# Kernel optimization log

Hardware: AMD Instinct MI355X
Metric: run time of the kernel (lower is better)

## Reference

```python
import jax, jax.numpy as jnp
import numpy as np

N = 50000
E = 800000
D = 16            # input_dim == hidden_dim == output_dim (required for consistency)
D2 = D * D
HEADS = 4
NEG_SLOPE = 0.2


def _gat_conv(x, src, dst, W, att_src, att_dst, bias):
    """PyG GATConv with concat=False (mean over heads), add_self_loops already applied.
    x: [N, Cin], W: [Cin, H*C], att_*: [H, C], bias: [C]."""
    H, C = att_src.shape
    xh = (x @ W).reshape(N, H, C)                     # [N, H, C]
    a_src = jnp.einsum('nhc,hc->nh', xh, att_src)      # [N, H]
    a_dst = jnp.einsum('nhc,hc->nh', xh, att_dst)
    alpha = jax.nn.leaky_relu(a_src[src] + a_dst[dst], NEG_SLOPE)   # [E, H]
    amax = jax.ops.segment_max(alpha, dst, num_segments=N)
    amax = jnp.where(jnp.isfinite(amax), amax, 0.0)
    ex = jnp.exp(alpha - jax.lax.stop_gradient(amax)[dst])
    denom = jax.ops.segment_sum(ex, dst, num_segments=N)
    coef = ex / (denom[dst] + 1e-16)                  # per-dst softmax over incoming edges
    acc = jnp.zeros((N, C), x.dtype)
    for h in range(H):  # loop over heads to avoid [E, H, C] intermediate
        acc = acc + jax.ops.segment_sum(coef[:, h:h + 1] * xh[src, h], dst, num_segments=N)
    return acc / H + bias


def setup_inputs() -> dict:
    key = jax.random.key(0)
    ks = jax.random.split(key, 20)
    s = lambda k, shape, fan: jax.random.normal(k, shape, jnp.float32) * (1.0 / np.sqrt(fan))
    inp = {
        'mean': jax.random.normal(ks[0], (N, D), jnp.float32),
        'cov': jax.random.normal(ks[1], (N, D, D), jnp.float32),
        'edge_index': jax.random.randint(ks[2], (2, E), 0, N, jnp.int32),
        # gat_mean params
        'W_mean': s(ks[3], (D, HEADS * D), D),
        'att_src_mean': s(ks[4], (HEADS, D), D),
        'att_dst_mean': s(ks[5], (HEADS, D), D),
        'bias_mean': jnp.zeros((D,), jnp.float32),
        # gat_cov params
        'W_cov': s(ks[6], (D2, HEADS * D2), D2),
        'att_src_cov': s(ks[7], (HEADS, D2), D2),
        'att_dst_cov': s(ks[8], (HEADS, D2), D2),
        'bias_cov': jnp.zeros((D2,), jnp.float32),
        # fc_mean: Linear(D,D) -> Linear(D,D)
        'fm_W1': s(ks[9], (D, D), D), 'fm_b1': jnp.zeros((D,), jnp.float32),
        'fm_W2': s(ks[10], (D, D), D), 'fm_b2': jnp.zeros((D,), jnp.float32),
        # fc_cov: Linear(D2,D2) -> Linear(D2,D2)
        'fcv_W1': s(ks[11], (D2, D2), D2), 'fcv_b1': jnp.zeros((D2,), jnp.float32),
        'fcv_W2': s(ks[12], (D2, D2), D2), 'fcv_b2': jnp.zeros((D2,), jnp.float32),
    }
    return inp


def reference(mean, cov, edge_index, W_mean, att_src_mean, att_dst_mean, bias_mean,
              W_cov, att_src_cov, att_dst_cov, bias_cov,
              fm_W1, fm_b1, fm_W2, fm_b2, fcv_W1, fcv_b1, fcv_W2, fcv_b2):
    loops = jnp.arange(N, dtype=edge_index.dtype)
    src = jnp.concatenate([edge_index[0], loops])
    dst = jnp.concatenate([edge_index[1], loops])

    cov_flat = cov.reshape(N, D2)
    mean_agg = _gat_conv(mean, src, dst, W_mean, att_src_mean, att_dst_mean, bias_mean)
    cov_agg = _gat_conv(cov_flat, src, dst, W_cov, att_src_cov, att_dst_cov, bias_cov)

    mean_out = (mean_agg @ fm_W1 + fm_b1) @ fm_W2 + fm_b2
    cov_out = (cov_agg @ fcv_W1 + fcv_b1) @ fcv_W2 + fcv_b2
    return mean_out, cov_out.reshape(N, D, D)
```

## Files before the change

kernel.cpp:

```cpp
#include <hip/hip_runtime.h>

#define NN 50000
#define EE 800000
#define DD 16
#define DD2 256
#define ETOT (EE + NN)
#define NB 196

typedef __bf16 bf16x8 __attribute__((ext_vector_type(8)));
typedef float f32x4 __attribute__((ext_vector_type(4)));
typedef float f32x2 __attribute__((ext_vector_type(2)));

__device__ inline unsigned short f2bf(float f) {
    unsigned int u = __float_as_uint(f);
    return (unsigned short)((u + 0x7FFFu + ((u >> 16) & 1u)) >> 16);
}

__device__ inline void gl2lds16(const void* g, void* l) {
    __builtin_amdgcn_global_load_lds((const __attribute__((address_space(1))) unsigned int*)g,
                                     (__attribute__((address_space(3))) unsigned int*)l, 16, 0, 0);
}

__global__ void k_count(const int* ei, int* counts) {
    int e = blockIdx.x * 256 + threadIdx.x;
    if (e < EE) atomicAdd(&counts[ei[EE + e]], 1);
}

__global__ void k_scan1(const int* counts, int* partial, int* bsum) {
    __shared__ int sh[256];
    int t = threadIdx.x;
    int n = blockIdx.x * 256 + t;
    int v = (n < NN) ? counts[n] + 1 : 0;
    sh[t] = v;
    __syncthreads();
    for (int d = 1; d < 256; d <<= 1) {
        int x = (t >= d) ? sh[t - d] : 0;
        __syncthreads();
        sh[t] += x;
        __syncthreads();
    }
    if (n < NN) partial[n] = sh[t];
    if (t == 255) bsum[blockIdx.x] = sh[255];
}

__global__ void k_scan3(const int* counts, const int* partial, const int* bsum,
                        int* row_start, int* cursor) {
    __shared__ int sh[256];
    int t = threadIdx.x;
    int v = (t < NB) ? bsum[t] : 0;
    sh[t] = v;
    __syncthreads();
    for (int d = 1; d < 256; d <<= 1) {
        int x = (t >= d) ? sh[t - d] : 0;
        __syncthreads();
        sh[t] += x;
        __syncthreads();
    }
    int boff = (blockIdx.x == 0) ? 0 : sh[blockIdx.x - 1];
    int n = blockIdx.x * 256 + t;
    if (n < NN) {
        int rs = partial[n] - (counts[n] + 1) + boff;
        row_start[n] = rs;
        cursor[n] = rs;
        if (n == NN - 1) row_start[NN] = partial[n] + boff;
    }
}

__global__ void k_scatter(const int* ei, int* cursor, int* srt) {
    int i = blockIdx.x * 256 + threadIdx.x;
    if (i >= ETOT) return;
    int s, d;
    if (i < EE) { s = ei[i]; d = ei[EE + i]; }
    else { s = d = i - EE; }
    int pos = atomicAdd(&cursor[d], 1);
    srt[pos] = s;
}

__global__ void k_pre(const float* fcv_W1, const float* fcv_W2, const float* fcv_b1, const float* fcv_b2,
                      const float* fm_W1, const float* fm_W2, const float* fm_b1, const float* fm_b2,
                      const float* W_cov, const float* as_cov, const float* ad_cov,
                      const float* W_mean, const float* as_mean, const float* ad_mean,
                      const float* bias_cov, const float* bias_mean,
                      unsigned short* WpT, float* bpc, float* vcov, float* vmean,
                      float* Wpm, float* bpm) {
    __shared__ float sh[256];
    int b = blockIdx.x, t = threadIdx.x;
    if (b < 1024) {
        int q = b >> 8, i = b & 255;
        const float* wrow = W_cov + (size_t)i * 1024 + q * 256;
        float t1 = 0.f;
        for (int j = 0; j < 256; ++j) t1 += wrow[j] * fcv_W1[j * 256 + t];
        sh[t] = t1;
        __syncthreads();
        float s = 0.f;
        for (int k = 0; k < 256; ++k) s += sh[k] * fcv_W2[k * 256 + t];
        int C = q * 32 + (i >> 3);
        int cs = C ^ (t & 7);
        WpT[(size_t)t * 1024 + cs * 8 + (i & 7)] = f2bf(0.25f * s);
    } else if (b == 1024) {
        float t1 = fcv_b1[t];
        for (int j = 0; j < 256; ++j) t1 += bias_cov[j] * fcv_W1[j * 256 + t];
        sh[t] = t1;
        __syncthreads();
        float s = fcv_b2[t];
        for (int k = 0; k < 256; ++k) s += sh[k] * fcv_W2[k * 256 + t];
        bpc[t] = s;
    } else if (b < 1033) {
        int ch = b - 1025, h = ch & 3;
        const float* att = (ch < 4) ? as_cov : ad_cov;
        int jl = t & 31, i8 = t >> 5;
        float av[8];
#pragma unroll
        for (int jj = 0; jj < 8; ++jj) av[jj] = att[h * 256 + jj * 32 + jl];
        for (int ii = 0; ii < 32; ++ii) {
            int i = ii * 8 + i8;
            const float* wr = W_cov + (size_t)i * 1024 + h * 256;
            float p = 0.f;
#pragma unroll
            for (int jj = 0; jj < 8; ++jj) p += wr[jj * 32 + jl] * av[jj];
#pragma unroll
            for (int off = 16; off; off >>= 1) p += __shfl_xor(p, off);
            if (jl == 0) vcov[ch * 256 + i] = p;
        }
    } else {
        {
            int j = t >> 4, c = t & 15;
            float s = 0.f;
            for (int k = 0; k < 16; ++k) s += fm_W1[j * 16 + k] * fm_W2[k * 16 + c];
            sh[j * 16 + c] = s;
        }
        if (t < 128) {
            int ch = t >> 4, i = t & 15, h = ch & 3;
            const float* att = (ch < 4) ? as_mean : ad_mean;
            float s = 0.f;
            for (int j = 0; j < 16; ++j) s += W_mean[i * 64 + h * 16 + j] * att[h * 16 + j];
            vmean[ch * 16 + i] = s;
        }
        __syncthreads();
#pragma unroll
        for (int r = 0; r < 4; ++r) {
            int idx = r * 256 + t;
            int k = idx >> 4, c = idx & 15, h = k >> 4, i = k & 15;
            float s = 0.f;
            for (int j = 0; j < 16; ++j) s += W_mean[i * 64 + h * 16 + j] * sh[j * 16 + c];
            Wpm[k * 16 + c] = 0.25f * s;
        }
        if (t < 16) {
            float b2 = fm_b2[t];
            for (int k = 0; k < 16; ++k) b2 += fm_b1[k] * fm_W2[k * 16 + t];
            float s = b2;
            for (int j = 0; j < 16; ++j) s += bias_mean[j] * sh[j * 16 + t];
            bpm[t] = s;
        }
    }
}

__global__ void __launch_bounds__(256) k_dots(const float* cov, const float* mean,
                                              const float* vcov, const float* vmean,
                                              float* asrc, float* adst, unsigned short* covb) {
    __shared__ float vc[8 * 256];
    __shared__ float vm[8 * 16];
    int t = threadIdx.x;
    for (int i = t; i < 2048; i += 256) vc[i] = vcov[i];
    if (t < 128) vm[t] = vmean[t];
    __syncthreads();
    int w = t >> 6, lane = t & 63;
    int n = blockIdx.x * 4 + w;
    float4 x = *(const float4*)(cov + (size_t)n * 256 + lane * 4);
    unsigned int u0 = (unsigned int)f2bf(x.x) | ((unsigned int)f2bf(x.y) << 16);
    unsigned int u1 = (unsigned int)f2bf(x.z) | ((unsigned int)f2bf(x.w) << 16);
    *(uint2*)((char*)covb + (size_t)n * 512 + lane * 8) = make_uint2(u0, u1);
    float p[8];
#pragma unroll
    for (int c = 0; c < 8; ++c) {
        float4 v = *(const float4*)&vc[c * 256 + lane * 4];
        p[c] = x.x * v.x + x.y * v.y + x.z * v.z + x.w * v.w;
    }
#pragma unroll
    for (int c = 0; c < 8; ++c)
        for (int off = 32; off; off >>= 1) p[c] += __shfl_xor(p[c], off);
    float xm = (lane < 16) ? mean[(size_t)n * 16 + lane] : 0.f;
    float q[8];
#pragma unroll
    for (int c = 0; c < 8; ++c) {
        q[c] = (lane < 16) ? xm * vm[c * 16 + lane] : 0.f;
        for (int off = 8; off; off >>= 1) q[c] += __shfl_xor(q[c], off);
    }
    if (lane == 0) {
        float4* ps = (float4*)(asrc + (size_t)n * 8);
        ps[0] = make_float4(p[0], p[1], p[2], p[3]);
        ps[1] = make_float4(q[0], q[1], q[2], q[3]);
        float4* pd = (float4*)(adst + (size_t)n * 8);
        pd[0] = make_float4(p[4], p[5], p[6], p[7]);
        pd[1] = make_float4(q[4], q[5], q[6], q[7]);
    }
}

__global__ void __launch_bounds__(256) k_agg(const int* __restrict__ row_start, const int* __restrict__ srt,
                                             const float* __restrict__ asrc, const float* __restrict__ adst,
                                             const unsigned short* __restrict__ covb, const float* __restrict__ mean,
                                             unsigned short* __restrict__ Ycat, float* __restrict__ Ym) {
    __shared__ float exbuf[4][64][8];
    int t = threadIdx.x;
    int w = t >> 6, lane = t & 63;
    int ml = lane & 15;
    int hl4 = lane >> 4;
    const char* covbc = (const char*)covb;
    const char* meanc = (const char*)mean;
    const char* asrcc = (const char*)asrc;
    unsigned lodc = (unsigned)lane << 3;
    unsigned lodm = (unsigned)ml << 2;

    for (int n = blockIdx.x * 4 + w; n < NN; n += gridDim.x * 4) {
        int beg = row_start[n], deg = row_start[n + 1] - beg;
        float ad[8];
        {
            const float4* pd = (const float4*)(adst + (size_t)n * 8);
            float4 d0 = pd[0], d1 = pd[1];
            ad[0] = d0.x; ad[1] = d0.y; ad[2] = d0.z; ad[3] = d0.w;
            ad[4] = d1.x; ad[5] = d1.y; ad[6] = d1.z; ad[7] = d1.w;
        }
        f32x2 acc[8];
#pragma unroll
        for (int k = 0; k < 8; ++k) acc[k] = (f32x2){0.f, 0.f};
        float accm = 0.f;
        float ds8[8] = {0, 0, 0, 0, 0, 0, 0, 0};

        auto loadg = [&](int jp, int s0v, uint2* cd, float* mv) {
            int se[4];
#pragma unroll
            for (int k2 = 0; k2 < 4; ++k2) se[k2] = __shfl(s0v, jp + k2);
#pragma unroll
            for (int k2 = 0; k2 < 4; ++k2) {
                cd[k2] = *(const uint2*)(covbc + (((unsigned)se[k2] << 9) + lodc));
                mv[k2] = *(const float*)(meanc + (((unsigned)se[k2] << 6) + lodm));
            }
        };
        auto compute4 = [&](int jp, const uint2* cd, const float* mv) {
#pragma unroll
            for (int k2 = 0; k2 < 4; ++k2) {
                float4 e0 = *(const float4*)&exbuf[w][jp + k2][0];
                float em = exbuf[w][jp + k2][4 + hl4];
                f32x2 x0 = (f32x2){__uint_as_float(cd[k2].x << 16), __uint_as_float(cd[k2].x & 0xffff0000u)};
                f32x2 x1 = (f32x2){__uint_as_float(cd[k2].y << 16), __uint_as_float(cd[k2].y & 0xffff0000u)};
                float ev[4] = {e0.x, e0.y, e0.z, e0.w};
#pragma unroll
                for (int h = 0; h < 4; ++h) {
                    f32x2 e2 = (f32x2){ev[h], ev[h]};
                    acc[h * 2 + 0] = __builtin_elementwise_fma(e2, x0, acc[h * 2 + 0]);
                    acc[h * 2 + 1] = __builtin_elementwise_fma(e2, x1, acc[h * 2 + 1]);
                }
                accm += em * mv[k2];
            }
        };

        for (int base = 0; base < deg; base += 64) {
            int i = base + lane;
            bool valid = i < deg;
            int s0 = srt[beg + (valid ? i : (deg - 1))];
            int cnt = min(64, deg - base);
            int cnt4 = (cnt + 3) & ~3;

            uint2 cdA[4], cdB[4];
            float mvA[4], mvB[4];
            loadg(0, s0, cdA, mvA);

            const float4* pa = (const float4*)(asrcc + ((size_t)((unsigned)s0 << 5)));
            float4 a0 = pa[0], a1 = pa[1];
            float av[8] = {a0.x, a0.y, a0.z, a0.w, a1.x, a1.y, a1.z, a1.w};
            float ex8[8];
#pragma unroll
            for (int c = 0; c < 8; ++c) {
                float al = av[c] + ad[c];
                al = (al >= 0.f) ? al : 0.2f * al;
                float e = __expf(al);
                e = valid ? e : 0.f;
                ex8[c] = e;
                ds8[c] += e;
            }
            *(float4*)&exbuf[w][lane][0] = make_float4(ex8[0], ex8[1], ex8[2], ex8[3]);
            *(float4*)&exbuf[w][lane][4] = make_float4(ex8[4], ex8[5], ex8[6], ex8[7]);

            for (int jp = 0; jp < cnt4; jp += 8) {
                bool hasB = (jp + 4) < cnt4;
                if (hasB) loadg(jp + 4, s0, cdB, mvB);
                compute4(jp, cdA, mvA);
                if (jp + 8 < cnt4) loadg(jp + 8, s0, cdA, mvA);
                if (hasB) compute4(jp + 4, cdB, mvB);
            }
        }
#pragma unroll
        for (int c = 0; c < 8; ++c)
            for (int off = 32; off; off >>= 1) ds8[c] += __shfl_xor(ds8[c], off);

        float invc[4] = {1.f / (ds8[0] + 1e-16f), 1.f / (ds8[1] + 1e-16f),
                         1.f / (ds8[2] + 1e-16f), 1.f / (ds8[3] + 1e-16f)};
        float dsm = (hl4 == 0) ? ds8[4] : (hl4 == 1) ? ds8[5] : (hl4 == 2) ? ds8[6] : ds8[7];
        float invm = 1.f / (dsm + 1e-16f);
        char* yrow = (char*)Ycat + (size_t)n * 2048;
        int cbase = lane >> 1, hl = lane & 1, sw = n & 7;
#pragma unroll
        for (int h = 0; h < 4; ++h) {
            float iv = invc[h];
            uint2 pk;
            pk.x = (unsigned int)f2bf(acc[h * 2 + 0].x * iv) | ((unsigned int)f2bf(acc[h * 2 + 0].y * iv) << 16);
            pk.y = (unsigned int)f2bf(acc[h * 2 + 1].x * iv) | ((unsigned int)f2bf(acc[h * 2 + 1].y * iv) << 16);
            int cs = (h * 32 + cbase) ^ sw;
            *(uint2*)(yrow + cs * 16 + hl * 8) = pk;
        }
        Ym[(size_t)n * 64 + lane] = accm * invm;
    }
}

__global__ void __launch_bounds__(256) k_gemm(const unsigned short* Ycat, const unsigned short* WpT,
                                              const float* bpc, float* out_cov,
                                              const float* Ym, const float* Wpm, const float* bpm,
                                              float* out_mean) {
    __shared__ __align__(16) unsigned short As[128 * 64];
    __shared__ __align__(16) unsigned short Bs[128 * 64];
    int t = threadIdx.x;
    if (blockIdx.x >= 782) {
        float* wm = (float*)As;
        float* bmv = (float*)Bs;
        for (int i = t; i < 1024; i += 256) wm[i] = Wpm[i];
        if (t < 16) bmv[t] = bpm[t];
        __syncthreads();
        int base = (blockIdx.x - 782) * 256;
        int c = t & 15;
#pragma unroll
        for (int p = 0; p < 16; ++p) {
            int node = base + p * 16 + (t >> 4);
            if (node < NN) {
                const float* yr = Ym + (size_t)node * 64;
                float s = bmv[c];
#pragma unroll
                for (int k = 0; k < 64; ++k) s += yr[k] * wm[k * 16 + c];
                out_mean[(size_t)node * 16 + c] = s;
            }
        }
        return;
    }
    int m0 = (blockIdx.x >> 1) * 128, c0 = (blockIdx.x & 1) * 128;
    int w = t >> 6, lane = t & 63;
    int mg = w >> 1, ng = w & 1;
    int q = lane >> 4, lm = lane & 15;
    f32x4 acc[4][4];
#pragma unroll
    for (int mt = 0; mt < 4; ++mt)
#pragma unroll
        for (int nt = 0; nt < 4; ++nt) acc[mt][nt] = (f32x4){0.f, 0.f, 0.f, 0.f};

    for (int kc = 0; kc < 16; ++kc) {
        int k0 = kc * 64;
#pragma unroll
        for (int i2 = 0; i2 < 4; ++i2) {
            int idx = t + i2 * 256;
            int row = idx >> 3, seg = idx & 7;
            int gm = m0 + row;
            if (gm < NN)
                gl2lds16(Ycat + (size_t)gm * 1024 + k0 + seg * 8, As + idx * 8);
        }
#pragma unroll
        for (int i2 = 0; i2 < 4; ++i2) {
            int idx = t + i2 * 256;
            int col = idx >> 3, seg = idx & 7;
            gl2lds16(WpT + (size_t)(c0 + col) * 1024 + k0 + seg * 8, Bs + idx * 8);
        }
        __syncthreads();
#pragma unroll
        for (int ks = 0; ks < 2; ++ks) {
            bf16x8 af[4], bfr[4];
#pragma unroll
            for (int mt = 0; mt < 4; ++mt) {
                int row = mg * 64 + mt * 16 + lm;
                int ch = (ks * 4 + q) ^ (row & 7);
                af[mt] = *(const bf16x8*)(As + row * 64 + ch * 8);
            }
#pragma unroll
            for (int nt = 0; nt < 4; ++nt) {
                int col = ng * 64 + nt * 16 + lm;
                int ch = (ks * 4 + q) ^ (col & 7);
                bfr[nt] = *(const bf16x8*)(Bs + col * 64 + ch * 8);
            }
#pragma unroll
            for (int mt = 0; mt < 4; ++mt)
#pragma unroll
                for (int nt = 0; nt < 4; ++nt)
                    acc[mt][nt] = __builtin_amdgcn_mfma_f32_16x16x32_bf16(af[mt], bfr[nt], acc[mt][nt], 0, 0, 0);
        }
        __syncthreads();
    }
#pragma unroll
    for (int nt = 0; nt < 4; ++nt) {
        int col = c0 + ng * 64 + nt * 16 + lm;
        float bias = bpc[col];
#pragma unroll
        for (int mt = 0; mt < 4; ++mt) {
#pragma unroll
            for (int e = 0; e < 4; ++e) {
                int r = m0 + mg * 64 + mt * 16 + q * 4 + e;
                if (r < NN)
                    __builtin_nontemporal_store(acc[mt][nt][e] + bias, &out_cov[(size_t)r * 256 + col]);
            }
        }
    }
}

extern "C" void kernel_launch(void* const* d_in, const int* in_sizes, int n_in,
                              void* d_out, int out_size, void* d_ws, size_t ws_size,
                              hipStream_t stream) {
    const float* mean = (const float*)d_in[0];
    const float* cov = (const float*)d_in[1];
    const int* ei = (const int*)d_in[2];
    const float* W_mean = (const float*)d_in[3];
    const float* as_mean = (const float*)d_in[4];
    const float* ad_mean = (const float*)d_in[5];
    const float* bias_mean = (const float*)d_in[6];
    const float* W_cov = (const float*)d_in[7];
    const float* as_cov = (const float*)d_in[8];
    const float* ad_cov = (const float*)d_in[9];
    const float* bias_cov = (const float*)d_in[10];
    const float* fm_W1 = (const float*)d_in[11];
    const float* fm_b1 = (const float*)d_in[12];
    const float* fm_W2 = (const float*)d_in[13];
    const float* fm_b2 = (const float*)d_in[14];
    const float* fcv_W1 = (const float*)d_in[15];
    const float* fcv_b1 = (const float*)d_in[16];
    const float* fcv_W2 = (const float*)d_in[17];
    const float* fcv_b2 = (const float*)d_in[18];

    float* out_mean = (float*)d_out;
    float* out_cov = (float*)d_out + (size_t)NN * DD;

    char* w = (char*)d_ws;
    auto alloc = [&](size_t bytes) -> void* {
        void* p = (void*)w;
        w += (bytes + 255) & ~(size_t)255;
        return p;
    };
    unsigned short* Ycat = (unsigned short*)alloc((size_t)NN * 1024 * 2);
    unsigned short* covb = (unsigned short*)alloc((size_t)NN * 256 * 2);
    float* Ym = (float*)alloc((size_t)NN * 64 * 4);
    int* counts = (int*)alloc(NN * 4);
    int* partial = (int*)alloc(NN * 4);
    int* bsum = (int*)alloc(256 * 4);
    int* row_start = (int*)alloc((NN + 1) * 4);
    int* cursor = (int*)alloc(NN * 4);
    int* srt = (int*)alloc((size_t)ETOT * 4);
    float* asrc = (float*)alloc((size_t)NN * 8 * 4);
    float* adst = (float*)alloc((size_t)NN * 8 * 4);
    float* vcov = (float*)alloc(8 * 256 * 4);
    float* vmean = (float*)alloc(8 * 16 * 4);
    unsigned short* WpT = (unsigned short*)alloc(256 * 1024 * 2);
    float* bpc = (float*)alloc(256 * 4);
    float* Wpm = (float*)alloc(64 * 16 * 4);
    float* bpm = (float*)alloc(16 * 4);

    hipMemsetAsync(counts, 0, NN * 4, stream);
    k_count<<<(EE + 255) / 256, 256, 0, stream>>>(ei, counts);
    k_scan1<<<NB, 256, 0, stream>>>(counts, partial, bsum);
    k_scan3<<<NB, 256, 0, stream>>>(counts, partial, bsum, row_start, cursor);
    k_scatter<<<(ETOT + 255) / 256, 256, 0, stream>>>(ei, cursor, srt);
    k_pre<<<1034, 256, 0, stream>>>(fcv_W1, fcv_W2, fcv_b1, fcv_b2, fm_W1, fm_W2, fm_b1, fm_b2,
                                    W_cov, as_cov, ad_cov, W_mean, as_mean, ad_mean,
                                    bias_cov, bias_mean, WpT, bpc, vcov, vmean, Wpm, bpm);
    k_dots<<<NN / 4, 256, 0, stream>>>(cov, mean, vcov, vmean, asrc, adst, covb);
    k_agg<<<2048, 256, 0, stream>>>(row_start, srt, asrc, adst, covb, mean, Ycat, Ym);
    k_gemm<<<782 + 196, 256, 0, stream>>>(Ycat, WpT, bpc, out_cov, Ym, Wpm, bpm, out_mean);
}
```

Measured before the change: 459.0 us.

## Stage gathered mean rows in LDS and restructure aggregation loop in k_agg

Each lane now loads its source node's full 64-byte mean row once with float4 loads and writes it into a swizzled LDS buffer. The per-edge 4-byte gathers of mean inside the inner loop go away. Softmax denominators are accumulated in the compute loop from LDS values, which replaces the end-of-node cross-lane shuffle reductions. The node index is made wave-uniform with readfirstlane, the cov-gather pipeline is double-buffered in groups of eight, launch bounds request 8 blocks per CU, and the grid shrinks to 1536 blocks. The costs are extra LDS per block and padding of the edge count to multiples of eight.

```diff
diff --git a/kernel.cpp b/kernel.cpp
--- a/kernel.cpp
+++ b/kernel.cpp
@@ -196,11 +196,12 @@
     }
 }
 
-__global__ void __launch_bounds__(256) k_agg(const int* __restrict__ row_start, const int* __restrict__ srt,
-                                             const float* __restrict__ asrc, const float* __restrict__ adst,
-                                             const unsigned short* __restrict__ covb, const float* __restrict__ mean,
-                                             unsigned short* __restrict__ Ycat, float* __restrict__ Ym) {
+__global__ void __launch_bounds__(256, 8) k_agg(const int* __restrict__ row_start, const int* __restrict__ srt,
+                                                const float* __restrict__ asrc, const float* __restrict__ adst,
+                                                const unsigned short* __restrict__ covb, const float* __restrict__ mean,
+                                                unsigned short* __restrict__ Ycat, float* __restrict__ Ym) {
     __shared__ float exbuf[4][64][8];
+    __shared__ float mrow[4][64][16];
     int t = threadIdx.x;
     int w = t >> 6, lane = t & 63;
     int ml = lane & 15;
@@ -209,38 +210,34 @@
     const char* meanc = (const char*)mean;
     const char* asrcc = (const char*)asrc;
     unsigned lodc = (unsigned)lane << 3;
-    unsigned lodm = (unsigned)ml << 2;
-
-    for (int n = blockIdx.x * 4 + w; n < NN; n += gridDim.x * 4) {
-        int beg = row_start[n], deg = row_start[n + 1] - beg;
-        float ad[8];
-        {
-            const float4* pd = (const float4*)(adst + (size_t)n * 8);
-            float4 d0 = pd[0], d1 = pd[1];
-            ad[0] = d0.x; ad[1] = d0.y; ad[2] = d0.z; ad[3] = d0.w;
-            ad[4] = d1.x; ad[5] = d1.y; ad[6] = d1.z; ad[7] = d1.w;
-        }
+    float* exw = &exbuf[w][0][0];
+    float* mrw = &mrow[w][0][0];
+
+    for (int n0 = blockIdx.x * 4; n0 < NN; n0 += gridDim.x * 4) {
+        int nu = __builtin_amdgcn_readfirstlane(n0 + w);
+        int beg = row_start[nu], deg = row_start[nu + 1] - beg;
+
         f32x2 acc[8];
 #pragma unroll
         for (int k = 0; k < 8; ++k) acc[k] = (f32x2){0.f, 0.f};
         float accm = 0.f;
-        float ds8[8] = {0, 0, 0, 0, 0, 0, 0, 0};
-
-        auto loadg = [&](int jp, int s0v, uint2* cd, float* mv) {
-            int se[4];
-#pragma unroll
-            for (int k2 = 0; k2 < 4; ++k2) se[k2] = __shfl(s0v, jp + k2);
+        float dsc[4] = {0, 0, 0, 0};
+        float dsm = 0.f;
+
+        auto loadg = [&](int jp, int s0v, uint2* cd) {
 #pragma unroll
             for (int k2 = 0; k2 < 4; ++k2) {
-                cd[k2] = *(const uint2*)(covbc + (((unsigned)se[k2] << 9) + lodc));
-                mv[k2] = *(const float*)(meanc + (((unsigned)se[k2] << 6) + lodm));
+                int se = __shfl(s0v, jp + k2);
+                cd[k2] = *(const uint2*)(covbc + (((unsigned)se << 9) + lodc));
             }
         };
-        auto compute4 = [&](int jp, const uint2* cd, const float* mv) {
+        auto compute4 = [&](int jp, const uint2* cd) {
 #pragma unroll
             for (int k2 = 0; k2 < 4; ++k2) {
-                float4 e0 = *(const float4*)&exbuf[w][jp + k2][0];
-                float em = exbuf[w][jp + k2][4 + hl4];
+                int e = jp + k2;
+                float4 e0 = *(const float4*)(exw + e * 8);
+                float em = exw[e * 8 + 4 + hl4];
+                float mv = mrw[e * 16 + (ml ^ ((e & 7) << 1))];
                 f32x2 x0 = (f32x2){__uint_as_float(cd[k2].x << 16), __uint_as_float(cd[k2].x & 0xffff0000u)};
                 f32x2 x1 = (f32x2){__uint_as_float(cd[k2].y << 16), __uint_as_float(cd[k2].y & 0xffff0000u)};
                 float ev[4] = {e0.x, e0.y, e0.z, e0.w};
@@ -250,7 +247,9 @@
                     acc[h * 2 + 0] = __builtin_elementwise_fma(e2, x0, acc[h * 2 + 0]);
                     acc[h * 2 + 1] = __builtin_elementwise_fma(e2, x1, acc[h * 2 + 1]);
                 }
-                accm += em * mv[k2];
+                dsc[0] += e0.x; dsc[1] += e0.y; dsc[2] += e0.z; dsc[3] += e0.w;
+                accm += em * mv;
+                dsm += em;
             }
         };
 
@@ -258,47 +257,61 @@
             int i = base + lane;
             bool valid = i < deg;
             int s0 = srt[beg + (valid ? i : (deg - 1))];
-            int cnt = min(64, deg - base);
-            int cnt4 = (cnt + 3) & ~3;
+            int cnt8 = (min(64, deg - base) + 7) & ~7;
 
             uint2 cdA[4], cdB[4];
-            float mvA[4], mvB[4];
-            loadg(0, s0, cdA, mvA);
-
-            const float4* pa = (const float4*)(asrcc + ((size_t)((unsigned)s0 << 5)));
-            float4 a0 = pa[0], a1 = pa[1];
-            float av[8] = {a0.x, a0.y, a0.z, a0.w, a1.x, a1.y, a1.z, a1.w};
-            float ex8[8];
-#pragma unroll
-            for (int c = 0; c < 8; ++c) {
-                float al = av[c] + ad[c];
-                al = (al >= 0.f) ? al : 0.2f * al;
-                float e = __expf(al);
-                e = valid ? e : 0.f;
-                ex8[c] = e;
-                ds8[c] += e;
-            }
-            *(float4*)&exbuf[w][lane][0] = make_float4(ex8[0], ex8[1], ex8[2], ex8[3]);
-            *(float4*)&exbuf[w][lane][4] = make_float4(ex8[4], ex8[5], ex8[6], ex8[7]);
-
-            for (int jp = 0; jp < cnt4; jp += 8) {
-                bool hasB = (jp + 4) < cnt4;
-                if (hasB) loadg(jp + 4, s0, cdB, mvB);
-                compute4(jp, cdA, mvA);
-                if (jp + 8 < cnt4) loadg(jp + 8, s0, cdA, mvA);
-                if (hasB) compute4(jp + 4, cdB, mvB);
-            }
-        }
-#pragma unroll
-        for (int c = 0; c < 8; ++c)
-            for (int off = 32; off; off >>= 1) ds8[c] += __shfl_xor(ds8[c], off);
-
-        float invc[4] = {1.f / (ds8[0] + 1e-16f), 1.f / (ds8[1] + 1e-16f),
-                         1.f / (ds8[2] + 1e-16f), 1.f / (ds8[3] + 1e-16f)};
-        float dsm = (hl4 == 0) ? ds8[4] : (hl4 == 1) ? ds8[5] : (hl4 == 2) ? ds8[6] : ds8[7];
+            loadg(0, s0, cdA);
+            loadg(4, s0, cdB);
+
+            {
+                const float4* pm = (const float4*)(meanc + ((size_t)((unsigned)s0 << 6)));
+                bool oddE = lane & 1;
+                int g0 = (lane >> 1) & 3;
+                float* mb = mrw + lane * 16;
+                float4 F0 = pm[0], F1 = pm[1];
+                float4 V0 = oddE ? make_float4(F0.z, F0.w, F0.x, F0.y) : F0;
+                float4 V1 = oddE ? make_float4(F1.z, F1.w, F1.x, F1.y) : F1;
+                *(float4*)(mb + ((0 ^ g0) << 2)) = V0;
+                *(float4*)(mb + ((1 ^ g0) << 2)) = V1;
+                float4 F2 = pm[2], F3 = pm[3];
+                float4 V2 = oddE ? make_float4(F2.z, F2.w, F2.x, F2.y) : F2;
+                float4 V3 = oddE ? make_float4(F3.z, F3.w, F3.x, F3.y) : F3;
+                *(float4*)(mb + ((2 ^ g0) << 2)) = V2;
+                *(float4*)(mb + ((3 ^ g0) << 2)) = V3;
+            }
+
+            {
+                const float4* pa = (const float4*)(asrcc + ((size_t)((unsigned)s0 << 5)));
+                float4 a0 = pa[0], a1 = pa[1];
+                const float4* pd = (const float4*)(adst + (size_t)nu * 8);
+                float4 d0 = pd[0], d1 = pd[1];
+                float av[8] = {a0.x, a0.y, a0.z, a0.w, a1.x, a1.y, a1.z, a1.w};
+                float ad[8] = {d0.x, d0.y, d0.z, d0.w, d1.x, d1.y, d1.z, d1.w};
+                float ex8[8];
+#pragma unroll
+                for (int c = 0; c < 8; ++c) {
+                    float al = av[c] + ad[c];
+                    al = (al >= 0.f) ? al : 0.2f * al;
+                    float e = __expf(al);
+                    ex8[c] = valid ? e : 0.f;
+                }
+                *(float4*)(exw + lane * 8) = make_float4(ex8[0], ex8[1], ex8[2], ex8[3]);
+                *(float4*)(exw + lane * 8 + 4) = make_float4(ex8[4], ex8[5], ex8[6], ex8[7]);
+            }
+
+            for (int jp = 0; jp < cnt8; jp += 8) {
+                compute4(jp, cdA);
+                if (jp + 8 < cnt8) loadg(jp + 8, s0, cdA);
+                compute4(jp + 4, cdB);
+                if (jp + 12 < cnt8) loadg(jp + 12, s0, cdB);
+            }
+        }
+
+        float invc[4] = {1.f / (dsc[0] + 1e-16f), 1.f / (dsc[1] + 1e-16f),
+                         1.f / (dsc[2] + 1e-16f), 1.f / (dsc[3] + 1e-16f)};
         float invm = 1.f / (dsm + 1e-16f);
-        char* yrow = (char*)Ycat + (size_t)n * 2048;
-        int cbase = lane >> 1, hl = lane & 1, sw = n & 7;
+        char* yrow = (char*)Ycat + (size_t)nu * 2048;
+        int cbase = lane >> 1, hl = lane & 1, sw = nu & 7;
 #pragma unroll
         for (int h = 0; h < 4; ++h) {
             float iv = invc[h];
@@ -308,7 +321,7 @@
             int cs = (h * 32 + cbase) ^ sw;
             *(uint2*)(yrow + cs * 16 + hl * 8) = pk;
         }
-        Ym[(size_t)n * 64 + lane] = accm * invm;
+        Ym[(size_t)nu * 64 + lane] = accm * invm;
     }
 }
 
@@ -465,6 +478,6 @@
                                     W_cov, as_cov, ad_cov, W_mean, as_mean, ad_mean,
                                     bias_cov, bias_mean, WpT, bpc, vcov, vmean, Wpm, bpm);
     k_dots<<<NN / 4, 256, 0, stream>>>(cov, mean, vcov, vmean, asrc, adst, covb);
-    k_agg<<<2048, 256, 0, stream>>>(row_start, srt, asrc, adst, covb, mean, Ycat, Ym);
+    k_agg<<<1536, 256, 0, stream>>>(row_start, srt, asrc, adst, covb, mean, Ycat, Ym);
     k_gemm<<<782 + 196, 256, 0, stream>>>(Ycat, WpT, bpc, out_cov, Ym, Wpm, bpm, out_mean);
 }
```

Result: no change. 453.3 us (-1.2%).
